# Performance work log

Measured on AMD Instinct MI355X. Metric: run time of the kernel, lower is better.

## Reference

```python
import jax, jax.numpy as jnp
import numpy as np

HIDDEN = 512
LAYERS = 3
K = 8
EPS = 1e-5


def build_adjacency(coords, k):
    # squared pairwise distances (monotone in cdist, so same top-k indices)
    sq = jnp.sum(coords * coords, axis=-1)                      # [B,N]
    d2 = sq[:, :, None] + sq[:, None, :] - 2.0 * jnp.einsum('bnc,bmc->bnm', coords, coords)
    _, idx = jax.lax.top_k(-d2, k + 1)                          # smallest k+1
    idx = idx[:, :, 1:]                                         # drop self  [B,N,k]
    B, N = coords.shape[:2]
    bidx = jnp.arange(B)[:, None, None]
    ridx = jnp.arange(N)[None, :, None]
    adj = jnp.zeros((B, N, N), coords.dtype).at[bidx, ridx, idx].set(1.0)
    adj = adj + jnp.swapaxes(adj, -2, -1)                       # symmetrize
    return (adj > 0).astype(coords.dtype)


def layer_norm(x, g, b):
    mu = jnp.mean(x, axis=-1, keepdims=True)
    var = jnp.var(x, axis=-1, keepdims=True)  # biased, matches torch LayerNorm
    return (x - mu) * jax.lax.rsqrt(var + EPS) * g + b


def setup_inputs() -> dict:
    key = jax.random.key(0)
    k1, k2, k3, k4 = jax.random.split(key, 4)
    B, N, H, L = 4, 4096, HIDDEN, LAYERS
    node_features = jax.random.normal(k1, (B, N, H), dtype=jnp.float32)
    coordinates = jax.random.uniform(k2, (B, N, 2), dtype=jnp.float32)
    scale = 1.0 / np.sqrt(H)
    W = jax.random.uniform(k3, (L, H, H), dtype=jnp.float32, minval=-scale, maxval=scale)
    b = jax.random.uniform(k4, (L, H), dtype=jnp.float32, minval=-scale, maxval=scale)
    gamma = jnp.ones((L, H), dtype=jnp.float32)
    beta = jnp.zeros((L, H), dtype=jnp.float32)
    return {"node_features": node_features, "coordinates": coordinates,
            "W": W, "b": b, "gamma": gamma, "beta": beta}


def reference(node_features, coordinates, W, b, gamma, beta):
    adj = build_adjacency(coordinates, K)                       # [B,N,N]
    x = node_features
    for i in range(LAYERS):
        x_new = jnp.einsum('bnm,bmh->bnh', adj, x)              # dense aggregate
        x_new = x_new @ W[i] + b[i]                             # linear
        x_new = jax.nn.relu(layer_norm(x_new, gamma[i], beta[i]))
        x = x + x_new if i > 0 else x_new
    return x
```

## Files before the change

### kernel.cpp

```cpp
#include <hip/hip_runtime.h>
#include <stdint.h>

#define HIDDEN 512
#define NLAYERS 3
#define KNN 8
#define CAP 64
#define EPSV 1e-5f
#define GRID 32
#define NCELL (GRID * GRID)

typedef unsigned long long u64;
typedef __attribute__((ext_vector_type(8))) short short8;
typedef __attribute__((ext_vector_type(4))) float f32x4;

#define GLL16(gp, lp)                                                         \
  __builtin_amdgcn_global_load_lds(                                           \
      (const __attribute__((address_space(1))) unsigned int*)(gp),            \
      (__attribute__((address_space(3))) unsigned int*)(lp), 16, 0, 0)

__device__ inline unsigned short f2bf(float x) {
  union { float f; unsigned u; } v; v.f = x;
  unsigned r = v.u + 0x7FFFu + ((v.u >> 16) & 1u);
  return (unsigned short)(r >> 16);
}
__device__ inline float bf2f(unsigned short u) {
  return __uint_as_float((unsigned)u << 16);
}

__global__ __launch_bounds__(1024) void grid_build_kernel(
    const float2* __restrict__ coords, int* __restrict__ cell_start,
    float2* __restrict__ scoord, int* __restrict__ sorig, int N) {
  __shared__ int hist[NCELL];
  __shared__ int offs[NCELL];
  int b = blockIdx.x;
  int t = threadIdx.x;
  hist[t] = 0;
  __syncthreads();
  const float2* cb = coords + (size_t)b * N;
  int mycell[4];
#pragma unroll
  for (int r = 0; r < 4; ++r) {
    int i = t + r * 1024;
    float2 c = cb[i];
    int cx = (int)(c.x * GRID); cx = cx < 0 ? 0 : (cx > GRID - 1 ? GRID - 1 : cx);
    int cy = (int)(c.y * GRID); cy = cy < 0 ? 0 : (cy > GRID - 1 ? GRID - 1 : cy);
    mycell[r] = cy * GRID + cx;
    atomicAdd(&hist[mycell[r]], 1);
  }
  __syncthreads();
  int v = hist[t];
  offs[t] = v;
  __syncthreads();
  for (int d = 1; d < NCELL; d <<= 1) {
    int add = (t >= d) ? offs[t - d] : 0;
    __syncthreads();
    offs[t] += add;
    __syncthreads();
  }
  int excl = offs[t] - v;
  cell_start[(size_t)b * (NCELL + 1) + t] = excl;
  if (t == 0) cell_start[(size_t)b * (NCELL + 1) + NCELL] = N;
  hist[t] = excl;
  __syncthreads();
#pragma unroll
  for (int r = 0; r < 4; ++r) {
    int i = t + r * 1024;
    int pos = atomicAdd(&hist[mycell[r]], 1);
    scoord[(size_t)b * N + pos] = cb[i];
    sorig[(size_t)b * N + pos] = i;
  }
}

__global__ __launch_bounds__(256) void knn_grid_kernel(
    const int* __restrict__ cell_start, const float2* __restrict__ scoord,
    const int* __restrict__ sorig, int* __restrict__ knn_s,
    int* __restrict__ cnt, int* __restrict__ rev, int N, int BN) {
  int gang = (blockIdx.x * blockDim.x + threadIdx.x) >> 3;
  int sub = threadIdx.x & 7;
  if (gang >= BN) return;
  int b = gang / N;
  float2 cn = scoord[gang];
  float sqn = __fmaf_rn(cn.y, cn.y, __fmul_rn(cn.x, cn.x));
  int cx = (int)(cn.x * GRID); cx = cx < 0 ? 0 : (cx > GRID - 1 ? GRID - 1 : cx);
  int cy = (int)(cn.y * GRID); cy = cy < 0 ? 0 : (cy > GRID - 1 ? GRID - 1 : cy);
  const int* cs = cell_start + (size_t)b * (NCELL + 1);
  const float2* sc = scoord + (size_t)b * N;
  const int* so = sorig + (size_t)b * N;

  u64 list[KNN + 1];
#pragma unroll
  for (int j = 0; j <= KNN; ++j) list[j] = ~0ull;

  auto scan_cell = [&](int ux, int uy) {
    int c = uy * GRID + ux;
    int s = cs[c], e = cs[c + 1];
    for (int p = s + sub; p < e; p += 8) {
      float2 cm = sc[p];
      float sqm = __fmaf_rn(cm.y, cm.y, __fmul_rn(cm.x, cm.x));
      float dot = __fmaf_rn(cn.y, cm.y, __fmul_rn(cn.x, cm.x));
      float d2 = __fsub_rn(__fadd_rn(sqn, sqm), __fmul_rn(2.0f, dot));
      unsigned ub = __float_as_uint(d2);
      unsigned k32 = (ub & 0x80000000u) ? ~ub : (ub | 0x80000000u);
      u64 key = ((u64)k32 << 24) | ((u64)(unsigned)so[p] << 12) | (u64)(unsigned)p;
      if (key < list[KNN]) {
        u64 cur = key;
#pragma unroll
        for (int j = 0; j <= KNN; ++j) {
          u64 lo = list[j] < cur ? list[j] : cur;
          u64 hi = list[j] < cur ? cur : list[j];
          list[j] = lo;
          cur = hi;
        }
      }
    }
  };

  for (int q = 0; q <= GRID; ++q) {
    if (q == 0) {
      scan_cell(cx, cy);
    } else {
      int x0 = cx - q, x1 = cx + q, y0 = cy - q, y1 = cy + q;
      int xa = x0 < 0 ? 0 : x0, xb_ = x1 > GRID - 1 ? GRID - 1 : x1;
      for (int ux = xa; ux <= xb_; ++ux) {
        if (y0 >= 0) scan_cell(ux, y0);
        if (y1 <= GRID - 1) scan_cell(ux, y1);
      }
      int ya = (y0 + 1) < 0 ? 0 : y0 + 1, yb = (y1 - 1) > GRID - 1 ? GRID - 1 : y1 - 1;
      for (int uy = ya; uy <= yb; ++uy) {
        if (x0 >= 0) scan_cell(x0, uy);
        if (x1 <= GRID - 1) scan_cell(x1, uy);
      }
      float bound = (float)q * (1.0f / GRID);
      float thr = bound * bound - 1e-5f;
      int cntn = 0;
#pragma unroll
      for (int j = 0; j <= KNN; ++j) {
        unsigned k32 = (unsigned)(list[j] >> 24);
        float d2v = (k32 >= 0x80000000u) ? __uint_as_float(k32 & 0x7FFFFFFFu)
                                         : -__uint_as_float(~k32);
        cntn += (list[j] != ~0ull && d2v < thr) ? 1 : 0;
      }
#pragma unroll
      for (int o = 1; o < 8; o <<= 1) cntn += __shfl_xor(cntn, o, 64);
      if (cntn >= 9) break;
    }
  }

  int gl = gang - b * N;
  for (int r = 0; r <= KNN; ++r) {
    u64 cand = list[0];
    u64 mn = cand;
#pragma unroll
    for (int o = 1; o < 8; o <<= 1) {
      u64 v = __shfl_xor(mn, o, 64);
      mn = v < mn ? v : mn;
    }
    if (cand == mn) {
#pragma unroll
      for (int j = 0; j < KNN; ++j) list[j] = list[j + 1];
      list[KNN] = ~0ull;
      if (r > 0) {
        int m = (int)(mn & 0xFFFull);
        knn_s[(size_t)gang * KNN + (r - 1)] = m;
        int gm = b * N + m;
        int pos = atomicAdd(&cnt[gm], 1);
        if (pos < CAP) rev[(size_t)gm * CAP + pos] = gl;
      }
    }
  }
}

__global__ __launch_bounds__(128) void x2bf_perm_kernel(const float* __restrict__ x,
                                                        const int* __restrict__ sorig,
                                                        unsigned short* __restrict__ xs,
                                                        int N) {
  int row = blockIdx.x;
  int b = row / N;
  int src = b * N + sorig[row];
  int t = threadIdx.x;
  float4 v = ((const float4*)(x + (size_t)src * HIDDEN))[t];
  ushort4 o;
  o.x = f2bf(v.x); o.y = f2bf(v.y); o.z = f2bf(v.z); o.w = f2bf(v.w);
  ((ushort4*)(xs + (size_t)row * HIDDEN))[t] = o;
}

__global__ __launch_bounds__(128) void agg_kernel(const unsigned short* __restrict__ x,
                                                  const int* __restrict__ knn,
                                                  const int* __restrict__ cnt,
                                                  const int* __restrict__ rev,
                                                  unsigned short* __restrict__ aggb,
                                                  int N) {
  int bn = blockIdx.x;
  int b = bn / N;
  int t = threadIdx.x;
  const int* my = knn + (size_t)bn * KNN;
  int nb[KNN];
#pragma unroll
  for (int j = 0; j < KNN; ++j) nb[j] = my[j];
  const unsigned short* xb = x + (size_t)b * N * HIDDEN;
  float4 acc = {0.f, 0.f, 0.f, 0.f};
#pragma unroll
  for (int j = 0; j < KNN; ++j) {
    ushort4 v = ((const ushort4*)(xb + (size_t)nb[j] * HIDDEN))[t];
    acc.x += bf2f(v.x); acc.y += bf2f(v.y); acc.z += bf2f(v.z); acc.w += bf2f(v.w);
  }
  int indeg = cnt[bn];
  if (indeg > CAP) indeg = CAP;
  const int* rv = rev + (size_t)bn * CAP;
  for (int i = 0; i < indeg; ++i) {
    int r = rv[i];
    bool dup = false;
#pragma unroll
    for (int j = 0; j < KNN; ++j) dup = dup || (r == nb[j]);
    if (!dup) {
      ushort4 v = ((const ushort4*)(xb + (size_t)r * HIDDEN))[t];
      acc.x += bf2f(v.x); acc.y += bf2f(v.y); acc.z += bf2f(v.z); acc.w += bf2f(v.w);
    }
  }
  ushort4 o;
  o.x = f2bf(acc.x); o.y = f2bf(acc.y); o.z = f2bf(acc.z); o.w = f2bf(acc.w);
  ((ushort4*)(aggb + (size_t)bn * HIDDEN))[t] = o;
}

__global__ __launch_bounds__(256) void wconv_kernel(const float* __restrict__ W,
                                                    unsigned short* __restrict__ Wt) {
  __shared__ unsigned short tile[64][65];
  int l = blockIdx.x >> 6;
  int t6 = blockIdx.x & 63;
  int k0 = (t6 >> 3) * 64, n0 = (t6 & 7) * 64;
  const float* Wl = W + (size_t)l * HIDDEN * HIDDEN;
  unsigned short* Wtl = Wt + (size_t)l * HIDDEN * HIDDEN;
  int t = threadIdx.x;
#pragma unroll
  for (int r = 0; r < 4; ++r) {
    int row = (t >> 4) + r * 16;
    int col = (t & 15) * 4;
    float4 v = *(const float4*)(Wl + (size_t)(k0 + row) * HIDDEN + n0 + col);
    tile[col + 0][row] = f2bf(v.x);
    tile[col + 1][row] = f2bf(v.y);
    tile[col + 2][row] = f2bf(v.z);
    tile[col + 3][row] = f2bf(v.w);
  }
  __syncthreads();
#pragma unroll
  for (int r = 0; r < 4; ++r) {
    int row = (t >> 4) + r * 16;
    int col = (t & 15) * 4;
    ushort4 o;
    o.x = tile[row][col + 0]; o.y = tile[row][col + 1];
    o.z = tile[row][col + 2]; o.w = tile[row][col + 3];
    *(ushort4*)(Wtl + (size_t)(n0 + row) * HIDDEN + k0 + col) = o;
  }
}

__global__ __launch_bounds__(256) void gemm_mfma_kernel(
    const unsigned short* __restrict__ A,
    const unsigned short* __restrict__ Wt,
    const float* __restrict__ bias,
    unsigned short* __restrict__ Cb) {
  __shared__ unsigned short As[128 * 32];
  __shared__ unsigned short Bs[128 * 32];
  int t = threadIdx.x;
  int n0 = blockIdx.x * 128;
  int m0 = blockIdx.y * 128;
  int w = t >> 6, lane = t & 63;
  int wr = w >> 1, wc = w & 1;
  int lm = lane & 15, q = lane >> 4;

  f32x4 acc[4][4];
#pragma unroll
  for (int i = 0; i < 4; ++i)
#pragma unroll
    for (int j = 0; j < 4; ++j) acc[i][j] = (f32x4){0.f, 0.f, 0.f, 0.f};

  int lrow = lane >> 2;
  int lcol = (lane & 3) * 8;
  int e0 = w, e1 = w + 4;

  const unsigned short* Arow0 = A + (size_t)(m0 + e0 * 16 + lrow) * HIDDEN + lcol;
  const unsigned short* Arow1 = A + (size_t)(m0 + e1 * 16 + lrow) * HIDDEN + lcol;
  const unsigned short* Brow0 = Wt + (size_t)(n0 + e0 * 16 + lrow) * HIDDEN + lcol;
  const unsigned short* Brow1 = Wt + (size_t)(n0 + e1 * 16 + lrow) * HIDDEN + lcol;

  for (int k0 = 0; k0 < HIDDEN; k0 += 32) {
    __syncthreads();
    GLL16(Arow0 + k0, As + e0 * 16 * 32);
    GLL16(Arow1 + k0, As + e1 * 16 * 32);
    GLL16(Brow0 + k0, Bs + e0 * 16 * 32);
    GLL16(Brow1 + k0, Bs + e1 * 16 * 32);
    __syncthreads();
    short8 af[4], bfr[4];
#pragma unroll
    for (int i = 0; i < 4; ++i)
      af[i] = *(const short8*)(As + (wr * 64 + i * 16 + lm) * 32 + q * 8);
#pragma unroll
    for (int j = 0; j < 4; ++j)
      bfr[j] = *(const short8*)(Bs + (wc * 64 + j * 16 + lm) * 32 + q * 8);
#pragma unroll
    for (int i = 0; i < 4; ++i)
#pragma unroll
      for (int j = 0; j < 4; ++j)
        acc[i][j] = __builtin_amdgcn_mfma_f32_16x16x32_bf16(af[i], bfr[j], acc[i][j], 0, 0, 0);
  }

#pragma unroll
  for (int i = 0; i < 4; ++i) {
    int row = m0 + wr * 64 + i * 16 + q * 4;
#pragma unroll
    for (int j = 0; j < 4; ++j) {
      int col = n0 + wc * 64 + j * 16 + lm;
      float bv = bias[col];
#pragma unroll
      for (int r = 0; r < 4; ++r)
        Cb[(size_t)(row + r) * HIDDEN + col] = f2bf(acc[i][j][r] + bv);
    }
  }
}

__global__ __launch_bounds__(256) void ln_relu_res_kernel(
    const unsigned short* __restrict__ tb, const float* __restrict__ g,
    const float* __restrict__ be, unsigned short* __restrict__ xs,
    float* __restrict__ out, const int* __restrict__ sorig,
    int N, int addres, int final_) {
  int row = (blockIdx.x << 2) + (threadIdx.x >> 6);
  int lane = threadIdx.x & 63;
  uint4 u = ((const uint4*)(tb + (size_t)row * HIDDEN))[lane];
  float v[8];
  v[0] = bf2f((unsigned short)(u.x & 0xFFFFu)); v[1] = bf2f((unsigned short)(u.x >> 16));
  v[2] = bf2f((unsigned short)(u.y & 0xFFFFu)); v[3] = bf2f((unsigned short)(u.y >> 16));
  v[4] = bf2f((unsigned short)(u.z & 0xFFFFu)); v[5] = bf2f((unsigned short)(u.z >> 16));
  v[6] = bf2f((unsigned short)(u.w & 0xFFFFu)); v[7] = bf2f((unsigned short)(u.w >> 16));
  float s = 0.f, ss = 0.f;
#pragma unroll
  for (int k = 0; k < 8; ++k) { s += v[k]; ss += v[k] * v[k]; }
#pragma unroll
  for (int o = 32; o > 0; o >>= 1) {
    s += __shfl_xor(s, o, 64);
    ss += __shfl_xor(ss, o, 64);
  }
  float mu = s * (1.0f / HIDDEN);
  float var = ss * (1.0f / HIDDEN) - mu * mu;
  float inv = rsqrtf(var + EPSV);
  float4 g0 = ((const float4*)g)[2 * lane], g1 = ((const float4*)g)[2 * lane + 1];
  float4 b0 = ((const float4*)be)[2 * lane], b1 = ((const float4*)be)[2 * lane + 1];
  float gv[8] = {g0.x, g0.y, g0.z, g0.w, g1.x, g1.y, g1.z, g1.w};
  float bv[8] = {b0.x, b0.y, b0.z, b0.w, b1.x, b1.y, b1.z, b1.w};
  float o8[8];
#pragma unroll
  for (int k = 0; k < 8; ++k)
    o8[k] = fmaxf((v[k] - mu) * inv * gv[k] + bv[k], 0.f);
  ushort4* xrow = (ushort4*)(xs + (size_t)row * HIDDEN);
  if (addres) {
    ushort4 r0 = xrow[2 * lane], r1 = xrow[2 * lane + 1];
    o8[0] += bf2f(r0.x); o8[1] += bf2f(r0.y); o8[2] += bf2f(r0.z); o8[3] += bf2f(r0.w);
    o8[4] += bf2f(r1.x); o8[5] += bf2f(r1.y); o8[6] += bf2f(r1.z); o8[7] += bf2f(r1.w);
  }
  if (final_) {
    int b = row / N;
    size_t dst = (size_t)(b * N + sorig[row]) * HIDDEN;
    float4 w0 = {o8[0], o8[1], o8[2], o8[3]};
    float4 w1 = {o8[4], o8[5], o8[6], o8[7]};
    ((float4*)(out + dst))[2 * lane] = w0;
    ((float4*)(out + dst))[2 * lane + 1] = w1;
  } else {
    ushort4 q0, q1;
    q0.x = f2bf(o8[0]); q0.y = f2bf(o8[1]); q0.z = f2bf(o8[2]); q0.w = f2bf(o8[3]);
    q1.x = f2bf(o8[4]); q1.y = f2bf(o8[5]); q1.z = f2bf(o8[6]); q1.w = f2bf(o8[7]);
    xrow[2 * lane] = q0;
    xrow[2 * lane + 1] = q1;
  }
}

extern "C" void kernel_launch(void* const* d_in, const int* in_sizes, int n_in,
                              void* d_out, int out_size, void* d_ws, size_t ws_size,
                              hipStream_t stream) {
  const float* nf = (const float*)d_in[0];
  const float2* coords = (const float2*)d_in[1];
  const float* Wall = (const float*)d_in[2];
  const float* ball = (const float*)d_in[3];
  const float* gall = (const float*)d_in[4];
  const float* beall = (const float*)d_in[5];
  float* out = (float*)d_out;

  int BN = in_sizes[0] / HIDDEN;
  int N = 4096;
  int B = BN / N;

  char* ws = (char*)d_ws;
  size_t off = 0;
  auto alloc = [&](size_t bytes) -> void* {
    off = (off + 255) & ~(size_t)255;
    void* p = ws + off;
    off += bytes;
    return p;
  };
  int* knn_s = (int*)alloc((size_t)BN * KNN * sizeof(int));
  int* cnt = (int*)alloc((size_t)BN * sizeof(int));
  int* rev = (int*)alloc((size_t)BN * CAP * sizeof(int));
  unsigned short* aggb = (unsigned short*)alloc((size_t)BN * HIDDEN * sizeof(unsigned short));
  unsigned short* tmpb = (unsigned short*)alloc((size_t)BN * HIDDEN * sizeof(unsigned short));
  unsigned short* Wt = (unsigned short*)alloc((size_t)NLAYERS * HIDDEN * HIDDEN * sizeof(unsigned short));
  unsigned short* xs = (unsigned short*)alloc((size_t)BN * HIDDEN * sizeof(unsigned short));
  int* cell_start = (int*)alloc((size_t)B * (NCELL + 1) * sizeof(int));
  float2* scoord = (float2*)alloc((size_t)BN * sizeof(float2));
  int* sorig = (int*)alloc((size_t)BN * sizeof(int));

  hipMemsetAsync(cnt, 0, (size_t)BN * sizeof(int), stream);
  grid_build_kernel<<<B, 1024, 0, stream>>>(coords, cell_start, scoord, sorig, N);
  knn_grid_kernel<<<(BN * 8 + 255) / 256, 256, 0, stream>>>(cell_start, scoord, sorig, knn_s, cnt, rev, N, BN);
  wconv_kernel<<<NLAYERS * 64, 256, 0, stream>>>(Wall, Wt);
  x2bf_perm_kernel<<<BN, 128, 0, stream>>>(nf, sorig, xs, N);

  for (int l = 0; l < NLAYERS; ++l) {
    agg_kernel<<<BN, 128, 0, stream>>>(xs, knn_s, cnt, rev, aggb, N);
    gemm_mfma_kernel<<<dim3(HIDDEN / 128, BN / 128), 256, 0, stream>>>(
        aggb, Wt + (size_t)l * HIDDEN * HIDDEN, ball + (size_t)l * HIDDEN, tmpb);
    ln_relu_res_kernel<<<BN / 4, 256, 0, stream>>>(
        tmpb, gall + (size_t)l * HIDDEN, beall + (size_t)l * HIDDEN,
        xs, out, sorig, N, l > 0, l == NLAYERS - 1);
  }
}
```

Baseline: 287.1 us.

## Fuse aggregation, GEMM, and LayerNorm/ReLU/residual into one per-layer kernel

Replaces the three per-layer kernels (gather aggregation, MFMA GEMM, LayerNorm+ReLU+residual) with one kernel per layer. Each 512-thread block aggregates 64 rows into a swizzled LDS tile, multiplies it by the full 512-wide weight matrix with MFMA, and does the row LayerNorm through a cross-wave LDS reduction before writing out. Ping-pong buffers xs/xs2 replace the in-place update. This is meant to remove the global round trips for the aggregated and pre-norm tensors and cut launch count. In exchange it uses about 64 KB of LDS for the A tile plus a 32 KB B tile, each thread holds a 64-float accumulator during aggregation, the epilogue uses strided scalar stores, and only 256 blocks are launched.

```diff
diff --git a/kernel.cpp b/kernel.cpp
--- a/kernel.cpp
+++ b/kernel.cpp
@@ -184,44 +184,6 @@
   ((ushort4*)(xs + (size_t)row * HIDDEN))[t] = o;
 }
 
-__global__ __launch_bounds__(128) void agg_kernel(const unsigned short* __restrict__ x,
-                                                  const int* __restrict__ knn,
-                                                  const int* __restrict__ cnt,
-                                                  const int* __restrict__ rev,
-                                                  unsigned short* __restrict__ aggb,
-                                                  int N) {
-  int bn = blockIdx.x;
-  int b = bn / N;
-  int t = threadIdx.x;
-  const int* my = knn + (size_t)bn * KNN;
-  int nb[KNN];
-#pragma unroll
-  for (int j = 0; j < KNN; ++j) nb[j] = my[j];
-  const unsigned short* xb = x + (size_t)b * N * HIDDEN;
-  float4 acc = {0.f, 0.f, 0.f, 0.f};
-#pragma unroll
-  for (int j = 0; j < KNN; ++j) {
-    ushort4 v = ((const ushort4*)(xb + (size_t)nb[j] * HIDDEN))[t];
-    acc.x += bf2f(v.x); acc.y += bf2f(v.y); acc.z += bf2f(v.z); acc.w += bf2f(v.w);
-  }
-  int indeg = cnt[bn];
-  if (indeg > CAP) indeg = CAP;
-  const int* rv = rev + (size_t)bn * CAP;
-  for (int i = 0; i < indeg; ++i) {
-    int r = rv[i];
-    bool dup = false;
-#pragma unroll
-    for (int j = 0; j < KNN; ++j) dup = dup || (r == nb[j]);
-    if (!dup) {
-      ushort4 v = ((const ushort4*)(xb + (size_t)r * HIDDEN))[t];
-      acc.x += bf2f(v.x); acc.y += bf2f(v.y); acc.z += bf2f(v.z); acc.w += bf2f(v.w);
-    }
-  }
-  ushort4 o;
-  o.x = f2bf(acc.x); o.y = f2bf(acc.y); o.z = f2bf(acc.z); o.w = f2bf(acc.w);
-  ((ushort4*)(aggb + (size_t)bn * HIDDEN))[t] = o;
-}
-
 __global__ __launch_bounds__(256) void wconv_kernel(const float* __restrict__ W,
                                                     unsigned short* __restrict__ Wt) {
   __shared__ unsigned short tile[64][65];
@@ -253,122 +215,176 @@
   }
 }
 
-__global__ __launch_bounds__(256) void gemm_mfma_kernel(
-    const unsigned short* __restrict__ A,
-    const unsigned short* __restrict__ Wt,
-    const float* __restrict__ bias,
-    unsigned short* __restrict__ Cb) {
-  __shared__ unsigned short As[128 * 32];
-  __shared__ unsigned short Bs[128 * 32];
+__global__ __launch_bounds__(512, 2) void layer_fused_kernel(
+    const unsigned short* __restrict__ xin,
+    const int* __restrict__ knn, const int* __restrict__ cnt,
+    const int* __restrict__ rev,
+    const unsigned short* __restrict__ Wl,
+    const float* __restrict__ bias, const float* __restrict__ gam,
+    const float* __restrict__ bet,
+    unsigned short* __restrict__ xout,
+    float* __restrict__ out, const int* __restrict__ sorig,
+    int N, int addres, int final_) {
+  __shared__ unsigned short aggA[64 * HIDDEN];
+  __shared__ unsigned short Bs[HIDDEN * 32];
+  __shared__ float red[8][64][2];
+  __shared__ float muv[64], invv[64];
+
   int t = threadIdx.x;
-  int n0 = blockIdx.x * 128;
-  int m0 = blockIdx.y * 128;
+  int m0 = blockIdx.x * 64;
+  int b = m0 / N;
+  const unsigned short* xb = xin + (size_t)b * N * HIDDEN;
+
+  {
+    int lr = t >> 3;
+    int cg = (t & 7) * 64;
+    int row = m0 + lr;
+    float acc[64];
+#pragma unroll
+    for (int e = 0; e < 64; ++e) acc[e] = 0.f;
+    const int* my = knn + (size_t)row * KNN;
+    int nb[KNN];
+#pragma unroll
+    for (int j = 0; j < KNN; ++j) nb[j] = my[j];
+
+    auto addrow = [&](const unsigned short* src) {
+#pragma unroll
+      for (int gq = 0; gq < 8; ++gq) {
+        uint4 u = *(const uint4*)(src + gq * 8);
+        acc[gq * 8 + 0] += bf2f((unsigned short)(u.x & 0xFFFFu));
+        acc[gq * 8 + 1] += bf2f((unsigned short)(u.x >> 16));
+        acc[gq * 8 + 2] += bf2f((unsigned short)(u.y & 0xFFFFu));
+        acc[gq * 8 + 3] += bf2f((unsigned short)(u.y >> 16));
+        acc[gq * 8 + 4] += bf2f((unsigned short)(u.z & 0xFFFFu));
+        acc[gq * 8 + 5] += bf2f((unsigned short)(u.z >> 16));
+        acc[gq * 8 + 6] += bf2f((unsigned short)(u.w & 0xFFFFu));
+        acc[gq * 8 + 7] += bf2f((unsigned short)(u.w >> 16));
+      }
+    };
+
+#pragma unroll
+    for (int j = 0; j < KNN; ++j)
+      addrow(xb + (size_t)nb[j] * HIDDEN + cg);
+
+    int indeg = cnt[row];
+    if (indeg > CAP) indeg = CAP;
+    const int* rv = rev + (size_t)row * CAP;
+    for (int i = 0; i < indeg; ++i) {
+      int r = rv[i];
+      bool dup = false;
+#pragma unroll
+      for (int j = 0; j < KNN; ++j) dup = dup || (r == nb[j]);
+      if (!dup) addrow(xb + (size_t)r * HIDDEN + cg);
+    }
+
+    int swz = (lr & 7) << 3;
+    unsigned short* arow = aggA + (size_t)lr * HIDDEN;
+#pragma unroll
+    for (int gq = 0; gq < 8; ++gq) {
+      int col = cg + gq * 8;
+      short8 p;
+#pragma unroll
+      for (int e = 0; e < 8; ++e) p[e] = (short)f2bf(acc[gq * 8 + e]);
+      *(short8*)(arow + (col ^ swz)) = p;
+    }
+  }
+
   int w = t >> 6, lane = t & 63;
-  int wr = w >> 1, wc = w & 1;
   int lm = lane & 15, q = lane >> 4;
-
-  f32x4 acc[4][4];
+  f32x4 cacc[4][4];
 #pragma unroll
   for (int i = 0; i < 4; ++i)
 #pragma unroll
-    for (int j = 0; j < 4; ++j) acc[i][j] = (f32x4){0.f, 0.f, 0.f, 0.f};
-
-  int lrow = lane >> 2;
-  int lcol = (lane & 3) * 8;
-  int e0 = w, e1 = w + 4;
-
-  const unsigned short* Arow0 = A + (size_t)(m0 + e0 * 16 + lrow) * HIDDEN + lcol;
-  const unsigned short* Arow1 = A + (size_t)(m0 + e1 * 16 + lrow) * HIDDEN + lcol;
-  const unsigned short* Brow0 = Wt + (size_t)(n0 + e0 * 16 + lrow) * HIDDEN + lcol;
-  const unsigned short* Brow1 = Wt + (size_t)(n0 + e1 * 16 + lrow) * HIDDEN + lcol;
+    for (int j = 0; j < 4; ++j) cacc[i][j] = (f32x4){0.f, 0.f, 0.f, 0.f};
 
   for (int k0 = 0; k0 < HIDDEN; k0 += 32) {
     __syncthreads();
-    GLL16(Arow0 + k0, As + e0 * 16 * 32);
-    GLL16(Arow1 + k0, As + e1 * 16 * 32);
-    GLL16(Brow0 + k0, Bs + e0 * 16 * 32);
-    GLL16(Brow1 + k0, Bs + e1 * 16 * 32);
+#pragma unroll
+    for (int cc = 0; cc < 4; ++cc) {
+      int d = (w * 4 + cc) * 64 + lane;
+      int n = d >> 2, s = d & 3;
+      GLL16(Wl + (size_t)n * HIDDEN + k0 + s * 8, Bs + (size_t)(w * 4 + cc) * 512);
+    }
     __syncthreads();
     short8 af[4], bfr[4];
 #pragma unroll
     for (int i = 0; i < 4; ++i)
-      af[i] = *(const short8*)(As + (wr * 64 + i * 16 + lm) * 32 + q * 8);
+      af[i] = *(const short8*)(aggA + (size_t)(i * 16 + lm) * HIDDEN +
+                               ((k0 + q * 8) ^ ((lm & 7) << 3)));
 #pragma unroll
     for (int j = 0; j < 4; ++j)
-      bfr[j] = *(const short8*)(Bs + (wc * 64 + j * 16 + lm) * 32 + q * 8);
+      bfr[j] = *(const short8*)(Bs + (size_t)(w * 64 + j * 16 + lm) * 32 + q * 8);
 #pragma unroll
     for (int i = 0; i < 4; ++i)
 #pragma unroll
       for (int j = 0; j < 4; ++j)
-        acc[i][j] = __builtin_amdgcn_mfma_f32_16x16x32_bf16(af[i], bfr[j], acc[i][j], 0, 0, 0);
-  }
-
-#pragma unroll
-  for (int i = 0; i < 4; ++i) {
-    int row = m0 + wr * 64 + i * 16 + q * 4;
-#pragma unroll
-    for (int j = 0; j < 4; ++j) {
-      int col = n0 + wc * 64 + j * 16 + lm;
-      float bv = bias[col];
+        cacc[i][j] = __builtin_amdgcn_mfma_f32_16x16x32_bf16(af[i], bfr[j], cacc[i][j], 0, 0, 0);
+  }
+
+  float bv[4], gv[4], bev[4];
+#pragma unroll
+  for (int j = 0; j < 4; ++j) {
+    int col = w * 64 + j * 16 + lm;
+    bv[j] = bias[col];
+    gv[j] = gam[col];
+    bev[j] = bet[col];
+  }
+  float vf[4][4][4];
+#pragma unroll
+  for (int i = 0; i < 4; ++i)
+#pragma unroll
+    for (int j = 0; j < 4; ++j)
 #pragma unroll
       for (int r = 0; r < 4; ++r)
-        Cb[(size_t)(row + r) * HIDDEN + col] = f2bf(acc[i][j][r] + bv);
-    }
-  }
-}
-
-__global__ __launch_bounds__(256) void ln_relu_res_kernel(
-    const unsigned short* __restrict__ tb, const float* __restrict__ g,
-    const float* __restrict__ be, unsigned short* __restrict__ xs,
-    float* __restrict__ out, const int* __restrict__ sorig,
-    int N, int addres, int final_) {
-  int row = (blockIdx.x << 2) + (threadIdx.x >> 6);
-  int lane = threadIdx.x & 63;
-  uint4 u = ((const uint4*)(tb + (size_t)row * HIDDEN))[lane];
-  float v[8];
-  v[0] = bf2f((unsigned short)(u.x & 0xFFFFu)); v[1] = bf2f((unsigned short)(u.x >> 16));
-  v[2] = bf2f((unsigned short)(u.y & 0xFFFFu)); v[3] = bf2f((unsigned short)(u.y >> 16));
-  v[4] = bf2f((unsigned short)(u.z & 0xFFFFu)); v[5] = bf2f((unsigned short)(u.z >> 16));
-  v[6] = bf2f((unsigned short)(u.w & 0xFFFFu)); v[7] = bf2f((unsigned short)(u.w >> 16));
-  float s = 0.f, ss = 0.f;
-#pragma unroll
-  for (int k = 0; k < 8; ++k) { s += v[k]; ss += v[k] * v[k]; }
-#pragma unroll
-  for (int o = 32; o > 0; o >>= 1) {
-    s += __shfl_xor(s, o, 64);
-    ss += __shfl_xor(ss, o, 64);
-  }
-  float mu = s * (1.0f / HIDDEN);
-  float var = ss * (1.0f / HIDDEN) - mu * mu;
-  float inv = rsqrtf(var + EPSV);
-  float4 g0 = ((const float4*)g)[2 * lane], g1 = ((const float4*)g)[2 * lane + 1];
-  float4 b0 = ((const float4*)be)[2 * lane], b1 = ((const float4*)be)[2 * lane + 1];
-  float gv[8] = {g0.x, g0.y, g0.z, g0.w, g1.x, g1.y, g1.z, g1.w};
-  float bv[8] = {b0.x, b0.y, b0.z, b0.w, b1.x, b1.y, b1.z, b1.w};
-  float o8[8];
-#pragma unroll
-  for (int k = 0; k < 8; ++k)
-    o8[k] = fmaxf((v[k] - mu) * inv * gv[k] + bv[k], 0.f);
-  ushort4* xrow = (ushort4*)(xs + (size_t)row * HIDDEN);
-  if (addres) {
-    ushort4 r0 = xrow[2 * lane], r1 = xrow[2 * lane + 1];
-    o8[0] += bf2f(r0.x); o8[1] += bf2f(r0.y); o8[2] += bf2f(r0.z); o8[3] += bf2f(r0.w);
-    o8[4] += bf2f(r1.x); o8[5] += bf2f(r1.y); o8[6] += bf2f(r1.z); o8[7] += bf2f(r1.w);
-  }
-  if (final_) {
-    int b = row / N;
-    size_t dst = (size_t)(b * N + sorig[row]) * HIDDEN;
-    float4 w0 = {o8[0], o8[1], o8[2], o8[3]};
-    float4 w1 = {o8[4], o8[5], o8[6], o8[7]};
-    ((float4*)(out + dst))[2 * lane] = w0;
-    ((float4*)(out + dst))[2 * lane + 1] = w1;
-  } else {
-    ushort4 q0, q1;
-    q0.x = f2bf(o8[0]); q0.y = f2bf(o8[1]); q0.z = f2bf(o8[2]); q0.w = f2bf(o8[3]);
-    q1.x = f2bf(o8[4]); q1.y = f2bf(o8[5]); q1.z = f2bf(o8[6]); q1.w = f2bf(o8[7]);
-    xrow[2 * lane] = q0;
-    xrow[2 * lane + 1] = q1;
-  }
+        vf[i][j][r] = bf2f(f2bf(cacc[i][j][r] + bv[j]));
+
+#pragma unroll
+  for (int i = 0; i < 4; ++i)
+#pragma unroll
+    for (int r = 0; r < 4; ++r) {
+      float sv = vf[i][0][r] + vf[i][1][r] + vf[i][2][r] + vf[i][3][r];
+      float sq = vf[i][0][r] * vf[i][0][r] + vf[i][1][r] * vf[i][1][r] +
+                 vf[i][2][r] * vf[i][2][r] + vf[i][3][r] * vf[i][3][r];
+#pragma unroll
+      for (int o = 1; o < 16; o <<= 1) {
+        sv += __shfl_xor(sv, o, 64);
+        sq += __shfl_xor(sq, o, 64);
+      }
+      if (lm == 0) {
+        int rr = i * 16 + q * 4 + r;
+        red[w][rr][0] = sv;
+        red[w][rr][1] = sq;
+      }
+    }
+  __syncthreads();
+  if (t < 64) {
+    float sv = 0.f, sq = 0.f;
+#pragma unroll
+    for (int ww = 0; ww < 8; ++ww) { sv += red[ww][t][0]; sq += red[ww][t][1]; }
+    float mu = sv * (1.0f / HIDDEN);
+    float var = sq * (1.0f / HIDDEN) - mu * mu;
+    muv[t] = mu;
+    invv[t] = rsqrtf(var + EPSV);
+  }
+  __syncthreads();
+
+#pragma unroll
+  for (int i = 0; i < 4; ++i)
+#pragma unroll
+    for (int r = 0; r < 4; ++r) {
+      int row = i * 16 + q * 4 + r;
+      int grow = m0 + row;
+      float mu = muv[row], inv = invv[row];
+      int so_ = final_ ? sorig[grow] : 0;
+#pragma unroll
+      for (int j = 0; j < 4; ++j) {
+        int col = w * 64 + j * 16 + lm;
+        float o = fmaxf((vf[i][j][r] - mu) * inv * gv[j] + bev[j], 0.f);
+        if (addres) o += bf2f(xin[(size_t)grow * HIDDEN + col]);
+        if (final_) out[(size_t)(b * N + so_) * HIDDEN + col] = o;
+        else        xout[(size_t)grow * HIDDEN + col] = f2bf(o);
+      }
+    }
 }
 
 extern "C" void kernel_launch(void* const* d_in, const int* in_sizes, int n_in,
@@ -397,10 +413,9 @@
   int* knn_s = (int*)alloc((size_t)BN * KNN * sizeof(int));
   int* cnt = (int*)alloc((size_t)BN * sizeof(int));
   int* rev = (int*)alloc((size_t)BN * CAP * sizeof(int));
-  unsigned short* aggb = (unsigned short*)alloc((size_t)BN * HIDDEN * sizeof(unsigned short));
-  unsigned short* tmpb = (unsigned short*)alloc((size_t)BN * HIDDEN * sizeof(unsigned short));
   unsigned short* Wt = (unsigned short*)alloc((size_t)NLAYERS * HIDDEN * HIDDEN * sizeof(unsigned short));
   unsigned short* xs = (unsigned short*)alloc((size_t)BN * HIDDEN * sizeof(unsigned short));
+  unsigned short* xs2 = (unsigned short*)alloc((size_t)BN * HIDDEN * sizeof(unsigned short));
   int* cell_start = (int*)alloc((size_t)B * (NCELL + 1) * sizeof(int));
   float2* scoord = (float2*)alloc((size_t)BN * sizeof(float2));
   int* sorig = (int*)alloc((size_t)BN * sizeof(int));
@@ -411,12 +426,15 @@
   wconv_kernel<<<NLAYERS * 64, 256, 0, stream>>>(Wall, Wt);
   x2bf_perm_kernel<<<BN, 128, 0, stream>>>(nf, sorig, xs, N);
 
-  for (int l = 0; l < NLAYERS; ++l) {
-    agg_kernel<<<BN, 128, 0, stream>>>(xs, knn_s, cnt, rev, aggb, N);
-    gemm_mfma_kernel<<<dim3(HIDDEN / 128, BN / 128), 256, 0, stream>>>(
-        aggb, Wt + (size_t)l * HIDDEN * HIDDEN, ball + (size_t)l * HIDDEN, tmpb);
-    ln_relu_res_kernel<<<BN / 4, 256, 0, stream>>>(
-        tmpb, gall + (size_t)l * HIDDEN, beall + (size_t)l * HIDDEN,
-        xs, out, sorig, N, l > 0, l == NLAYERS - 1);
-  }
-}
+  layer_fused_kernel<<<BN / 64, 512, 0, stream>>>(
+      xs, knn_s, cnt, rev, Wt, ball, gall, beall,
+      xs2, out, sorig, N, 0, 0);
+  layer_fused_kernel<<<BN / 64, 512, 0, stream>>>(
+      xs2, knn_s, cnt, rev, Wt + (size_t)1 * HIDDEN * HIDDEN,
+      ball + HIDDEN, gall + HIDDEN, beall + HIDDEN,
+      xs, out, sorig, N, 1, 0);
+  layer_fused_kernel<<<BN / 64, 512, 0, stream>>>(
+      xs, knn_s, cnt, rev, Wt + (size_t)2 * HIDDEN * HIDDEN,
+      ball + 2 * HIDDEN, gall + 2 * HIDDEN, beall + 2 * HIDDEN,
+      xs2 , out, sorig, N, 1, 1);
+}
```

After: 437.8 us. 1.52x slower.
